# Optimization experiments

Hardware: AMD Instinct MI355X
Metric: run time of the kernel (lower is better)

Reference implementation:

```python
import jax, jax.numpy as jnp
import numpy as np

D_MODEL = 1024
N_HEADS = 16
D_K = D_MODEL // N_HEADS
D_FF = 4096
EPS = 1e-5


def _layernorm(x, g, b):
    mu = jnp.mean(x, axis=-1, keepdims=True)
    var = jnp.var(x, axis=-1, keepdims=True)
    return (x - mu) * jax.lax.rsqrt(var + EPS) * g + b


def setup_inputs() -> dict:
    key = jax.random.key(0)
    ks = jax.random.split(key, 12)
    s = 0.02
    x = jax.random.normal(ks[0], (2, 2048, D_MODEL), dtype=jnp.float32)
    # Linear weights stored [in, out] so y = x @ W + b
    wq = jax.random.normal(ks[1], (D_MODEL, D_MODEL), dtype=jnp.float32) * s
    wk = jax.random.normal(ks[2], (D_MODEL, D_MODEL), dtype=jnp.float32) * s
    wv = jax.random.normal(ks[3], (D_MODEL, D_MODEL), dtype=jnp.float32) * s
    wo = jax.random.normal(ks[4], (D_MODEL, D_MODEL), dtype=jnp.float32) * s
    bq = jnp.zeros((D_MODEL,), jnp.float32)
    bk = jnp.zeros((D_MODEL,), jnp.float32)
    bv = jnp.zeros((D_MODEL,), jnp.float32)
    bo = jnp.zeros((D_MODEL,), jnp.float32)
    ln1_g = jnp.ones((D_MODEL,), jnp.float32)
    ln1_b = jnp.zeros((D_MODEL,), jnp.float32)
    ln2_g = jnp.ones((D_MODEL,), jnp.float32)
    ln2_b = jnp.zeros((D_MODEL,), jnp.float32)
    w1 = jax.random.normal(ks[5], (D_MODEL, D_FF), dtype=jnp.float32) * s
    b1 = jnp.zeros((D_FF,), jnp.float32)
    w2 = jax.random.normal(ks[6], (D_FF, D_MODEL), dtype=jnp.float32) * s
    b2 = jnp.zeros((D_MODEL,), jnp.float32)
    return {"x": x, "wq": wq, "bq": bq, "wk": wk, "bk": bk, "wv": wv, "bv": bv,
            "wo": wo, "bo": bo, "ln1_g": ln1_g, "ln1_b": ln1_b,
            "ln2_g": ln2_g, "ln2_b": ln2_b, "w1": w1, "b1": b1, "w2": w2, "b2": b2}


def reference(x, wq, bq, wk, bk, wv, bv, wo, bo, ln1_g, ln1_b, ln2_g, ln2_b, w1, b1, w2, b2):
    B, S, _ = x.shape
    res = x
    # project and split heads: [B, S, H, Dk]
    q = (x @ wq + bq).reshape(B, S, N_HEADS, D_K)
    k = (x @ wk + bk).reshape(B, S, N_HEADS, D_K)
    v = (x @ wv + bv).reshape(B, S, N_HEADS, D_K)
    # full score matrix [B, H, Sq, Sk] (faithful to unfused original)
    scores = jnp.einsum('bqhd,bkhd->bhqk', q, k) / jnp.sqrt(jnp.float32(D_K))
    weights = jax.nn.softmax(scores, axis=-1)
    attn = jnp.einsum('bhqk,bkhd->bqhd', weights, v).reshape(B, S, D_MODEL)
    x = _layernorm(res + attn @ wo + bo, ln1_g, ln1_b)
    res = x
    h = jax.nn.relu(x @ w1 + b1)
    x = _layernorm(res + h @ w2 + b2, ln2_g, ln2_b)
    return x
```

## Files before the change

kernel.cpp:

```cpp
#include <hip/hip_runtime.h>
#include <hip/hip_bf16.h>
#include <stdint.h>


typedef __hip_bfloat16 bf16;
typedef short bf16x8 __attribute__((ext_vector_type(8)));
typedef float f32x4 __attribute__((ext_vector_type(4)));

#if __has_builtin(__builtin_amdgcn_exp2f)
#define EXP2F(x) __builtin_amdgcn_exp2f(x)
#else
#define EXP2F(x) exp2f(x)
#endif

__device__ __forceinline__ float bf2f_lo(unsigned u) { return __uint_as_float(u << 16); }
__device__ __forceinline__ float bf2f_hi(unsigned u) { return __uint_as_float(u & 0xffff0000u); }
__device__ __forceinline__ ushort f2bf(float f) {
  union { bf16 h; ushort u; } c; c.h = __float2bfloat16(f); return c.u;
}
__device__ __forceinline__ uint pk_bf16(float a, float b) {
  union { __hip_bfloat162 h2; uint u; } c;
  c.h2 = __float22bfloat162_rn(make_float2(a, b));
  return c.u;
}
__device__ __forceinline__ bool is_f32(const uint* probe) { return probe[0] == 0x3F800000u; }
__device__ __forceinline__ float ld_param(const void* p, size_t i, bool f32) {
  return f32 ? ((const float*)p)[i] : __bfloat162float(((const bf16*)p)[i]);
}

template <bool A_EXT, bool RES_EXT>
__device__ __forceinline__ void gemm_body(
    const void* __restrict__ Av, const ushort* __restrict__ BT,
    const void* __restrict__ bias, const void* __restrict__ res,
    void* __restrict__ C, int N_, int K_, int bm, int bn,
    int kb, int ke, int mode, const uint* probe) {
  __shared__ ushort Asm_[128 * 32];
  __shared__ ushort Bsm_[128 * 32];

  const bool F32 = is_f32(probe);
  const bool AF = A_EXT && F32;

  const int tid = threadIdx.x;
  const int wave = tid >> 6;
  const int lane = tid & 63;
  const int wm = wave & 1, wn = wave >> 1;

  const int r0 = tid >> 2;
  const int c0 = (tid & 3) * 8;
  const int dA0 = r0 * 32 + c0;
  const int dA1 = dA0 + 64 * 32;

  const size_t aRow0 = (size_t)(bm * 128 + r0) * K_;
  const size_t aRow1 = aRow0 + (size_t)64 * K_;
  const ushort* pB0 = BT + (size_t)(bn * 128 + r0) * K_ + c0;
  const ushort* pB1 = pB0 + (size_t)64 * K_;

  auto ld4 = [&](int kk, uint4& A0, uint4& A1, uint4& B0, uint4& B1) {
    if (AF) {
      const float* Af = (const float*)Av;
      const float4 f0 = *(const float4*)(Af + aRow0 + kk + c0);
      const float4 f1 = *(const float4*)(Af + aRow0 + kk + c0 + 4);
      const float4 g0 = *(const float4*)(Af + aRow1 + kk + c0);
      const float4 g1 = *(const float4*)(Af + aRow1 + kk + c0 + 4);
      A0.x = pk_bf16(f0.x, f0.y); A0.y = pk_bf16(f0.z, f0.w);
      A0.z = pk_bf16(f1.x, f1.y); A0.w = pk_bf16(f1.z, f1.w);
      A1.x = pk_bf16(g0.x, g0.y); A1.y = pk_bf16(g0.z, g0.w);
      A1.z = pk_bf16(g1.x, g1.y); A1.w = pk_bf16(g1.z, g1.w);
    } else {
      const ushort* Ab = (const ushort*)Av;
      A0 = *(const uint4*)(Ab + aRow0 + kk + c0);
      A1 = *(const uint4*)(Ab + aRow1 + kk + c0);
    }
    B0 = *(const uint4*)(pB0 + kk);
    B1 = *(const uint4*)(pB1 + kk);
  };

  f32x4 zero = {0.f, 0.f, 0.f, 0.f};
  f32x4 acc[4][4];
#pragma unroll
  for (int i = 0; i < 4; ++i)
#pragma unroll
    for (int j = 0; j < 4; ++j) acc[i][j] = zero;

  const int m16 = lane & 15;
  const int quad = lane >> 4;
  const int koff = quad * 8;

  uint4 a0, a1, b0, b1;
  ld4(kb, a0, a1, b0, b1);

  for (int k0 = kb; k0 < ke; k0 += 32) {
    __syncthreads();
    *(uint4*)&Asm_[dA0] = a0;
    *(uint4*)&Asm_[dA1] = a1;
    *(uint4*)&Bsm_[dA0] = b0;
    *(uint4*)&Bsm_[dA1] = b1;
    __syncthreads();

    if (k0 + 32 < ke) ld4(k0 + 32, a0, a1, b0, b1);

    bf16x8 af[4], bfr[4];
#pragma unroll
    for (int i = 0; i < 4; ++i)
      af[i] = *(const bf16x8*)&Asm_[(wm * 64 + i * 16 + m16) * 32 + koff];
#pragma unroll
    for (int j = 0; j < 4; ++j)
      bfr[j] = *(const bf16x8*)&Bsm_[(wn * 64 + j * 16 + m16) * 32 + koff];
#pragma unroll
    for (int i = 0; i < 4; ++i)
#pragma unroll
      for (int j = 0; j < 4; ++j)
        acc[i][j] = __builtin_amdgcn_mfma_f32_16x16x32_bf16(af[i], bfr[j], acc[i][j], 0, 0, 0);
  }

  const int row0 = bm * 128 + wm * 64;
  const int col0 = bn * 128 + wn * 64;
#pragma unroll
  for (int j = 0; j < 4; ++j) {
    const int col = col0 + j * 16 + m16;
    const float bv = (mode == 3) ? 0.f : ld_param(bias, col, F32);
#pragma unroll
    for (int i = 0; i < 4; ++i) {
#pragma unroll
      for (int r = 0; r < 4; ++r) {
        const int row = row0 + i * 16 + quad * 4 + r;
        float v = acc[i][j][r] + bv;
        if (mode == 1) v = fmaxf(v, 0.f);
        if (mode == 2) v += ld_param(res, (size_t)row * N_ + col, RES_EXT && F32);
        if (mode >= 2) ((float*)C)[(size_t)row * N_ + col] = v;
        else ((bf16*)C)[(size_t)row * N_ + col] = __float2bfloat16(v);
      }
    }
  }
}

__global__ __launch_bounds__(256) void gemm_qkv(
    const void* A, const ushort* BT0, const ushort* BT1, const ushort* BT2,
    const void* b0, const void* b1, const void* b2,
    bf16* C0, bf16* C1, bf16* C2, const uint* probe) {
  const int sel = blockIdx.y >> 3, bn = blockIdx.y & 7;
  const ushort* BT = sel == 0 ? BT0 : (sel == 1 ? BT1 : BT2);
  const void* bb = sel == 0 ? b0 : (sel == 1 ? b1 : b2);
  bf16* C = sel == 0 ? C0 : (sel == 1 ? C1 : C2);
  gemm_body<true, false>(A, BT, bb, nullptr, C, 1024, 1024, blockIdx.x, bn,
                         0, 1024, 0, probe);
}
__global__ __launch_bounds__(256) void gemm_wo_sk(
    const ushort* A, const ushort* BT, const void* bias, const void* res,
    float* C0, float* C1, const uint* probe) {
  const int kz = blockIdx.z;
  gemm_body<false, true>(A, BT, bias, res, kz ? C1 : C0, 1024, 1024,
                         blockIdx.x, blockIdx.y, kz * 512, kz * 512 + 512,
                         kz ? 3 : 2, probe);
}
__global__ __launch_bounds__(256) void gemm_ffn1(
    const ushort* A, const ushort* BT, const void* bias, bf16* C, const uint* probe) {
  gemm_body<false, false>(A, BT, bias, nullptr, C, 4096, 1024,
                          blockIdx.x, blockIdx.y, 0, 1024, 1, probe);
}
__global__ __launch_bounds__(256) void gemm_ffn2_sk(
    const ushort* A, const ushort* BT, const void* bias, const ushort* res,
    float* C0, float* C1, const uint* probe) {
  const int kz = blockIdx.z;
  gemm_body<false, false>(A, BT, bias, res, kz ? C1 : C0, 1024, 4096,
                          blockIdx.x, blockIdx.y, kz * 2048, kz * 2048 + 2048,
                          kz ? 3 : 2, probe);
}

__global__ __launch_bounds__(256) void transpose_all(
    const void* W0, const void* W1, const void* W2, const void* W3,
    const void* W4, const void* W5,
    ushort* D0, ushort* D1, ushort* D2, ushort* D3, ushort* D4, ushort* D5,
    const uint* probe) {
  const int z = blockIdx.z;
  if (z < 4 && blockIdx.x >= 32) return;
  int n0, k0, K_, N_;
  const void* W;
  ushort* D;
  if (z < 4) {
    n0 = blockIdx.x * 32; k0 = blockIdx.y * 32; K_ = 1024; N_ = 1024;
    W = z == 0 ? W0 : z == 1 ? W1 : z == 2 ? W2 : W3;
    D = z == 0 ? D0 : z == 1 ? D1 : z == 2 ? D2 : D3;
  } else if (z == 4) {
    n0 = blockIdx.x * 32; k0 = blockIdx.y * 32; K_ = 1024; N_ = 4096; W = W4; D = D4;
  } else {
    n0 = blockIdx.y * 32; k0 = blockIdx.x * 32; K_ = 4096; N_ = 1024; W = W5; D = D5;
  }
  const bool F32 = is_f32(probe);
  __shared__ ushort tile[32][33];
  const int tx = threadIdx.x & 31, ty = threadIdx.x >> 5;
#pragma unroll
  for (int i = 0; i < 32; i += 8) {
    const size_t src = (size_t)(k0 + ty + i) * N_ + n0 + tx;
    tile[ty + i][tx] = F32 ? f2bf(((const float*)W)[src]) : ((const ushort*)W)[src];
  }
  __syncthreads();
#pragma unroll
  for (int i = 0; i < 32; i += 8)
    D[(size_t)(n0 + ty + i) * K_ + k0 + tx] = tile[tx][ty + i];
}

template <bool OUT_EXT>
__global__ __launch_bounds__(256) void ln_kernel(
    const float* __restrict__ X, const float* __restrict__ P,
    const void* __restrict__ g, const void* __restrict__ bta,
    void* __restrict__ out, const uint* probe) {
  const bool F32 = is_f32(probe);
  const int row = blockIdx.x;
  const int tid = threadIdx.x;
  const float4 a = *(const float4*)(X + (size_t)row * 1024 + tid * 4);
  const float4 b = *(const float4*)(P + (size_t)row * 1024 + tid * 4);
  const float xv[4] = {a.x + b.x, a.y + b.y, a.z + b.z, a.w + b.w};
  float s = xv[0] + xv[1] + xv[2] + xv[3];
  float ss = xv[0] * xv[0] + xv[1] * xv[1] + xv[2] * xv[2] + xv[3] * xv[3];
#pragma unroll
  for (int o = 32; o > 0; o >>= 1) { s += __shfl_down(s, o); ss += __shfl_down(ss, o); }
  __shared__ float red[8];
  if ((tid & 63) == 0) { red[tid >> 6] = s; red[4 + (tid >> 6)] = ss; }
  __syncthreads();
  s = red[0] + red[1] + red[2] + red[3];
  ss = red[4] + red[5] + red[6] + red[7];
  const float mu = s * (1.f / 1024.f);
  const float rstd = rsqrtf(ss * (1.f / 1024.f) - mu * mu + 1e-5f);
#pragma unroll
  for (int i = 0; i < 4; ++i) {
    const size_t idx = (size_t)row * 1024 + tid * 4 + i;
    const float y = (xv[i] - mu) * rstd * ld_param(g, tid * 4 + i, F32) +
                    ld_param(bta, tid * 4 + i, F32);
    if (OUT_EXT && F32) ((float*)out)[idx] = y;
    else ((bf16*)out)[idx] = __float2bfloat16(y);
  }
}

__global__ __launch_bounds__(256) void attn_mfma(
    const ushort* __restrict__ Qm, const ushort* __restrict__ Km,
    const ushort* __restrict__ Vm, ushort* __restrict__ Om) {
  __shared__ ushort Ks[64 * 72];
  __shared__ ushort Vt[64 * 72];
  __shared__ ushort Pw[4][32 * 72];

  const int tid = threadIdx.x;
  const int wave = tid >> 6, lane = tid & 63;
  const int m16 = lane & 15, quad = lane >> 4;
  const int bb = blockIdx.z, h = blockIdx.y;
  const size_t hb = ((size_t)bb * 2048) * 1024 + h * 64;
  const int q0 = blockIdx.x * 128 + wave * 32;

  const float QS = 0.125f * 1.44269504f;
  bf16x8 qf[2][2];
#pragma unroll
  for (int i = 0; i < 2; ++i)
#pragma unroll
    for (int c = 0; c < 2; ++c) {
      const uint4 u = *(const uint4*)(Qm + hb + (size_t)(q0 + 16 * i + m16) * 1024 + c * 32 + quad * 8);
      const uint w[4] = {u.x, u.y, u.z, u.w};
      bf16x8 f;
#pragma unroll
      for (int j = 0; j < 4; ++j) {
        const uint p = pk_bf16(bf2f_lo(w[j]) * QS, bf2f_hi(w[j]) * QS);
        f[2 * j]     = (short)(p & 0xffffu);
        f[2 * j + 1] = (short)(p >> 16);
      }
      qf[i][c] = f;
    }

  f32x4 zero = {0.f, 0.f, 0.f, 0.f};
  f32x4 acc[2][4];
#pragma unroll
  for (int i = 0; i < 2; ++i)
#pragma unroll
    for (int j = 0; j < 4; ++j) acc[i][j] = zero;
  float lp[2][4] = {{0.f, 0.f, 0.f, 0.f}, {0.f, 0.f, 0.f, 0.f}};

  const int skey = tid >> 2;
  const int sd = (tid & 3) * 8;
  const int pp = tid & 31;
  const int dc = tid >> 5;
  const int ka_ = 16 * ((2 * pp) & 3) + ((2 * pp) >> 2);
  const int kb_ = 16 * ((2 * pp + 1) & 3) + ((2 * pp + 1) >> 2);
  const ushort* Kg = Km + hb;
  const ushort* Vg = Vm + hb;

  uint4 kr0, kr1, vr0, vr1;
  kr0 = *(const uint4*)(Kg + (size_t)skey * 1024 + sd);
  kr1 = *(const uint4*)(Kg + (size_t)skey * 1024 + sd + 32);
  vr0 = *(const uint4*)(Vg + (size_t)ka_ * 1024 + dc * 8);
  vr1 = *(const uint4*)(Vg + (size_t)kb_ * 1024 + dc * 8);

  for (int kt = 0; kt < 2048; kt += 64) {
    __syncthreads();
    *(uint4*)&Ks[skey * 72 + sd] = kr0;
    *(uint4*)&Ks[skey * 72 + sd + 32] = kr1;
    {
      const uint va[4] = {vr0.x, vr0.y, vr0.z, vr0.w};
      const uint vb[4] = {vr1.x, vr1.y, vr1.z, vr1.w};
#pragma unroll
      for (int j = 0; j < 8; ++j) {
        const uint lo = (j & 1) ? (va[j >> 1] >> 16) : (va[j >> 1] & 0xffffu);
        const uint hi = (j & 1) ? (vb[j >> 1] & 0xffff0000u) : (vb[j >> 1] << 16);
        *(uint*)&Vt[(dc * 8 + j) * 72 + 2 * pp] = lo | hi;
      }
    }
    __syncthreads();

    if (kt + 64 < 2048) {
      kr0 = *(const uint4*)(Kg + (size_t)(kt + 64 + skey) * 1024 + sd);
      kr1 = *(const uint4*)(Kg + (size_t)(kt + 64 + skey) * 1024 + sd + 32);
      vr0 = *(const uint4*)(Vg + (size_t)(kt + 64 + ka_) * 1024 + dc * 8);
      vr1 = *(const uint4*)(Vg + (size_t)(kt + 64 + kb_) * 1024 + dc * 8);
    }

    f32x4 s[2][4];
#pragma unroll
    for (int i = 0; i < 2; ++i)
#pragma unroll
      for (int jn = 0; jn < 4; ++jn) s[i][jn] = zero;
#pragma unroll
    for (int c = 0; c < 2; ++c) {
      bf16x8 kb4[4];
#pragma unroll
      for (int jn = 0; jn < 4; ++jn)
        kb4[jn] = *(const bf16x8*)&Ks[(jn * 16 + m16) * 72 + c * 32 + quad * 8];
#pragma unroll
      for (int i = 0; i < 2; ++i)
#pragma unroll
        for (int jn = 0; jn < 4; ++jn)
          s[i][jn] = __builtin_amdgcn_mfma_f32_16x16x32_bf16(qf[i][c], kb4[jn], s[i][jn], 0, 0, 0);
    }

#pragma unroll
    for (int i = 0; i < 2; ++i)
#pragma unroll
      for (int r = 0; r < 4; ++r) {
        const float p0 = EXP2F(s[i][0][r]);
        const float p1 = EXP2F(s[i][1][r]);
        const float p2 = EXP2F(s[i][2][r]);
        const float p3 = EXP2F(s[i][3][r]);
        lp[i][r] += (p0 + p1) + (p2 + p3);
        uint2 pk;
        pk.x = pk_bf16(p0, p1);
        pk.y = pk_bf16(p2, p3);
        *(uint2*)&Pw[wave][(16 * i + quad * 4 + r) * 72 + m16 * 4] = pk;
      }
    asm volatile("s_waitcnt lgkmcnt(0)" ::: "memory");

#pragma unroll
    for (int c = 0; c < 2; ++c) {
      bf16x8 pa[2], vb4[4];
#pragma unroll
      for (int i = 0; i < 2; ++i)
        pa[i] = *(const bf16x8*)&Pw[wave][(16 * i + m16) * 72 + c * 32 + quad * 8];
#pragma unroll
      for (int jd = 0; jd < 4; ++jd)
        vb4[jd] = *(const bf16x8*)&Vt[(jd * 16 + m16) * 72 + c * 32 + quad * 8];
#pragma unroll
      for (int i = 0; i < 2; ++i)
#pragma unroll
        for (int jd = 0; jd < 4; ++jd)
          acc[i][jd] = __builtin_amdgcn_mfma_f32_16x16x32_bf16(pa[i], vb4[jd], acc[i][jd], 0, 0, 0);
    }
  }

#pragma unroll
  for (int i = 0; i < 2; ++i)
#pragma unroll
    for (int r = 0; r < 4; ++r) {
      float l = lp[i][r];
      l += __shfl_xor(l, 1); l += __shfl_xor(l, 2);
      l += __shfl_xor(l, 4); l += __shfl_xor(l, 8);
      const float inv = 1.f / l;
      const size_t rowoff = hb + (size_t)(q0 + 16 * i + quad * 4 + r) * 1024;
#pragma unroll
      for (int jd = 0; jd < 4; ++jd)
        Om[rowoff + jd * 16 + m16] = f2bf(acc[i][jd][r] * inv);
    }
}

extern "C" void kernel_launch(void* const* d_in, const int* in_sizes, int n_in,
                              void* d_out, int out_size, void* d_ws, size_t ws_size,
                              hipStream_t stream) {
  const void* x   = d_in[0];
  const void* wq  = d_in[1];
  const void* bq  = d_in[2];
  const void* wk  = d_in[3];
  const void* bk  = d_in[4];
  const void* wv  = d_in[5];
  const void* bv  = d_in[6];
  const void* wo  = d_in[7];
  const void* bo  = d_in[8];
  const uint* probe = (const uint*)d_in[9];
  const void* ln1g = d_in[9];
  const void* ln1b = d_in[10];
  const void* ln2g = d_in[11];
  const void* ln2b = d_in[12];
  const void* w1  = d_in[13];
  const void* b1  = d_in[14];
  const void* w2  = d_in[15];
  const void* b2  = d_in[16];

  char* ws = (char*)d_ws;
  const size_t MB = 1ull << 20;
  ushort* wqT = (ushort*)(ws + 0 * MB);
  ushort* wkT = (ushort*)(ws + 2 * MB);
  ushort* wvT = (ushort*)(ws + 4 * MB);
  ushort* woT = (ushort*)(ws + 6 * MB);
  ushort* w1T = (ushort*)(ws + 8 * MB);
  ushort* w2T = (ushort*)(ws + 16 * MB);
  ushort* Qb  = (ushort*)(ws + 24 * MB);
  ushort* Kb  = (ushort*)(ws + 32 * MB);
  ushort* Vb  = (ushort*)(ws + 40 * MB);
  ushort* AO  = (ushort*)(ws + 72 * MB);
  float*  T1  = (float*)(ws + 24 * MB);
  float*  P1w = (float*)(ws + 40 * MB);
  ushort* X1  = (ushort*)(ws + 56 * MB);
  ushort* Hb  = (ushort*)(ws + 24 * MB);
  float*  T1b = (float*)(ws + 0 * MB);
  float*  P1b = (float*)(ws + 64 * MB);

  const dim3 blk(256);
  transpose_all<<<dim3(128, 32, 6), blk, 0, stream>>>(
      wq, wk, wv, wo, w1, w2, wqT, wkT, wvT, woT, w1T, w2T, probe);

  gemm_qkv<<<dim3(32, 24), blk, 0, stream>>>(x, wqT, wkT, wvT, bq, bk, bv,
                                             (bf16*)Qb, (bf16*)Kb, (bf16*)Vb, probe);
  attn_mfma<<<dim3(16, 16, 2), blk, 0, stream>>>(Qb, Kb, Vb, AO);
  gemm_wo_sk<<<dim3(32, 8, 2), blk, 0, stream>>>(AO, woT, bo, x, T1, P1w, probe);
  ln_kernel<false><<<dim3(4096), blk, 0, stream>>>(T1, P1w, ln1g, ln1b, X1, probe);
  gemm_ffn1<<<dim3(32, 32), blk, 0, stream>>>(X1, w1T, b1, (bf16*)Hb, probe);
  gemm_ffn2_sk<<<dim3(32, 8, 2), blk, 0, stream>>>(Hb, w2T, b2, X1, T1b, P1b, probe);
  ln_kernel<true><<<dim3(4096), blk, 0, stream>>>(T1b, P1b, ln2g, ln2b, d_out, probe);
}
```

Measured before the change: 397.9 us.

## Replace 128-tile GEMMs with 256x256 LDS-DMA pipelined GEMM kernel

Adds a 512-thread GEMM that computes a 256x256 output tile per block, stages A/B tiles into double-buffered swizzled LDS via global_load_lds, and interleaves the next-stage loads with MFMA 16x16x32 bursts under raised wave priority. QKV, FFN1 and FFN2 now use it. The QKV input is pre-converted to bf16 by a new convert_x kernel so the GEMM reads only bf16. The larger tiles raise data reuse and the hand pipelining hides load latency. In exchange there are far fewer blocks (e.g. 192 for QKV, 128 for FFN2), which may underfill the CUs, plus one extra launch.

```diff
diff --git a/kernel.cpp b/kernel.cpp
--- a/kernel.cpp
+++ b/kernel.cpp
@@ -26,6 +26,166 @@
 __device__ __forceinline__ bool is_f32(const uint* probe) { return probe[0] == 0x3F800000u; }
 __device__ __forceinline__ float ld_param(const void* p, size_t i, bool f32) {
   return f32 ? ((const float*)p)[i] : __bfloat162float(((const bf16*)p)[i]);
+}
+
+__device__ __forceinline__ void barrier_raw() {
+  asm volatile("" ::: "memory");
+  __builtin_amdgcn_s_barrier();
+  asm volatile("" ::: "memory");
+}
+__device__ __forceinline__ void lgkm0() {
+  asm volatile("s_waitcnt lgkmcnt(0)" ::: "memory");
+}
+__device__ __forceinline__ void glds16(const ushort* g, ushort* l) {
+  __builtin_amdgcn_global_load_lds(
+      (const __attribute__((address_space(1))) void*)g,
+      (__attribute__((address_space(3))) void*)l, 16, 0, 0);
+}
+
+#define MFMA16(MH, NH)                                                        \
+  do {                                                                        \
+    _Pragma("unroll") for (int c_ = 0; c_ < 2; ++c_)                          \
+    _Pragma("unroll") for (int fi_ = 0; fi_ < 4; ++fi_)                       \
+    _Pragma("unroll") for (int gi_ = 0; gi_ < 2; ++gi_)                       \
+      acc[(MH) * 4 + fi_][(NH) * 2 + gi_] =                                   \
+          __builtin_amdgcn_mfma_f32_16x16x32_bf16(                            \
+              areg[fi_][c_], breg[(NH) * 2 + gi_][c_],                        \
+              acc[(MH) * 4 + fi_][(NH) * 2 + gi_], 0, 0, 0);                  \
+  } while (0)
+
+__device__ __forceinline__ void gemm256_body(
+    const ushort* __restrict__ A, const ushort* __restrict__ BT,
+    const void* __restrict__ bias, const void* __restrict__ res,
+    void* __restrict__ C, int N_, int K_, int bm, int bn,
+    int kb, int ke, int mode, const uint* probe) {
+  __shared__ ushort As[2][16384];
+  __shared__ ushort Bs[2][16384];
+
+  const int tid = threadIdx.x;
+  const int wave = tid >> 6;
+  const int lane = tid & 63;
+  const int wm = wave >> 2;
+  const int wn = wave & 3;
+  const int m16 = lane & 15;
+  const int quad = lane >> 4;
+  const int nt = (ke - kb) >> 6;
+
+  const int srow = lane >> 2;
+  const int skc = ((lane & 3) * 8) ^ (((lane >> 5) & 1) << 4);
+  const ushort* pA = A + (size_t)(bm * 256 + wave * 16 + srow) * K_ + kb + skc;
+  const ushort* pB = BT + (size_t)(bn * 256 + wave * 16 + srow) * K_ + kb + skc;
+  const size_t hstep = (size_t)128 * K_;
+  ushort* dA = &As[0][0] + wave * 1024;
+  ushort* dB = &Bs[0][0] + wave * 1024;
+
+  auto stageA = [&](int b, int half, int t) {
+    const ushort* g = pA + (size_t)half * hstep + t * 64;
+    ushort* d = dA + b * 16384 + half * 8192;
+    glds16(g, d);
+    glds16(g + 32, d + 512);
+  };
+  auto stageB = [&](int b, int half, int t) {
+    const ushort* g = pB + (size_t)half * hstep + t * 64;
+    ushort* d = dB + b * 16384 + half * 8192;
+    glds16(g, d);
+    glds16(g + 32, d + 512);
+  };
+
+  const int fr_off = m16 * 32 + ((quad * 8) ^ (((m16 >> 3) & 1) << 4));
+  const ushort* rA = &As[0][0] + fr_off;
+  const ushort* rB = &Bs[0][0] + fr_off;
+  auto ldA = [&](int b, int f, int c) {
+    return *(const bf16x8*)(rA + b * 16384 +
+                            ((f >> 2) * 8 + wm * 4 + (f & 3)) * 1024 + c * 512);
+  };
+  auto ldB = [&](int b, int g, int c) {
+    return *(const bf16x8*)(rB + b * 16384 +
+                            ((g >> 1) * 8 + wn * 2 + (g & 1)) * 1024 + c * 512);
+  };
+
+  f32x4 acc[8][4];
+#pragma unroll
+  for (int f = 0; f < 8; ++f)
+#pragma unroll
+    for (int g = 0; g < 4; ++g) acc[f][g] = (f32x4){0.f, 0.f, 0.f, 0.f};
+  bf16x8 areg[4][2], breg[4][2];
+
+  stageA(0, 0, 0); stageB(0, 0, 0); stageA(0, 1, 0); stageB(0, 1, 0);
+  if (nt > 1) { stageA(1, 0, 1); stageB(1, 0, 1); }
+  asm volatile("s_waitcnt vmcnt(4)" ::: "memory");
+  barrier_raw();
+
+  for (int t = 0; t < nt; ++t) {
+    const int b = t & 1, bo = b ^ 1;
+#pragma unroll
+    for (int fi = 0; fi < 4; ++fi) { areg[fi][0] = ldA(b, fi, 0); areg[fi][1] = ldA(b, fi, 1); }
+#pragma unroll
+    for (int gi = 0; gi < 2; ++gi) { breg[gi][0] = ldB(b, gi, 0); breg[gi][1] = ldB(b, gi, 1); }
+    if (t + 1 < nt) stageA(bo, 1, t + 1);
+    barrier_raw(); lgkm0();
+    __builtin_amdgcn_s_setprio(1); MFMA16(0, 0); __builtin_amdgcn_s_setprio(0);
+    barrier_raw();
+#pragma unroll
+    for (int gi = 2; gi < 4; ++gi) { breg[gi][0] = ldB(b, gi, 0); breg[gi][1] = ldB(b, gi, 1); }
+    if (t + 1 < nt) stageB(bo, 1, t + 1);
+    barrier_raw(); lgkm0();
+    __builtin_amdgcn_s_setprio(1); MFMA16(0, 1); __builtin_amdgcn_s_setprio(0);
+    barrier_raw();
+#pragma unroll
+    for (int fi = 0; fi < 4; ++fi) { areg[fi][0] = ldA(b, fi + 4, 0); areg[fi][1] = ldA(b, fi + 4, 1); }
+    if (t + 2 < nt) stageA(b, 0, t + 2);
+    barrier_raw(); lgkm0();
+    __builtin_amdgcn_s_setprio(1); MFMA16(1, 0); __builtin_amdgcn_s_setprio(0);
+    barrier_raw();
+    if (t + 2 < nt) stageB(b, 0, t + 2);
+    barrier_raw(); lgkm0();
+    __builtin_amdgcn_s_setprio(1); MFMA16(1, 1); __builtin_amdgcn_s_setprio(0);
+    if (t + 2 < nt) asm volatile("s_waitcnt vmcnt(4)" ::: "memory");
+    else            asm volatile("s_waitcnt vmcnt(0)" ::: "memory");
+    barrier_raw();
+  }
+
+  const bool F32 = is_f32(probe);
+#pragma unroll
+  for (int g = 0; g < 4; ++g) {
+    const int col = bn * 256 + (g >> 1) * 128 + wn * 32 + (g & 1) * 16 + m16;
+    const float bv = (mode == 3) ? 0.f : ld_param(bias, col, F32);
+#pragma unroll
+    for (int f = 0; f < 8; ++f) {
+      const int rowb = bm * 256 + (f >> 2) * 128 + wm * 64 + (f & 3) * 16 + quad * 4;
+#pragma unroll
+      for (int r = 0; r < 4; ++r) {
+        const int row = rowb + r;
+        float v = acc[f][g][r] + bv;
+        if (mode == 1) v = fmaxf(v, 0.f);
+        if (mode == 2) v += __bfloat162float(((const bf16*)res)[(size_t)row * N_ + col]);
+        if (mode >= 2) ((float*)C)[(size_t)row * N_ + col] = v;
+        else ((bf16*)C)[(size_t)row * N_ + col] = __float2bfloat16(v);
+      }
+    }
+  }
+}
+
+__global__ __launch_bounds__(512, 2) void gemm256_qkv(
+    const ushort* A, const ushort* BT0, const ushort* BT1, const ushort* BT2,
+    const void* b0, const void* b1, const void* b2,
+    bf16* C0, bf16* C1, bf16* C2, const uint* probe) {
+  const int sel = blockIdx.y >> 2, bn = blockIdx.y & 3;
+  const ushort* BT = sel == 0 ? BT0 : (sel == 1 ? BT1 : BT2);
+  const void* bb = sel == 0 ? b0 : (sel == 1 ? b1 : b2);
+  bf16* C = sel == 0 ? C0 : (sel == 1 ? C1 : C2);
+  gemm256_body(A, BT, bb, nullptr, C, 1024, 1024, blockIdx.x, bn, 0, 1024, 0, probe);
+}
+__global__ __launch_bounds__(512, 2) void gemm256_ffn1(
+    const ushort* A, const ushort* BT, const void* bias, bf16* C, const uint* probe) {
+  gemm256_body(A, BT, bias, nullptr, C, 4096, 1024, blockIdx.x, blockIdx.y, 0, 1024, 1, probe);
+}
+__global__ __launch_bounds__(512, 2) void gemm256_ffn2_sk(
+    const ushort* A, const ushort* BT, const void* bias, const ushort* res,
+    float* C0, float* C1, const uint* probe) {
+  const int kz = blockIdx.z;
+  gemm256_body(A, BT, bias, res, kz ? (void*)C1 : (void*)C0, 1024, 4096,
+               blockIdx.x, blockIdx.y, kz * 2048, kz * 2048 + 2048, kz ? 3 : 2, probe);
 }
 
 template <bool A_EXT, bool RES_EXT>
@@ -134,17 +294,6 @@
   }
 }
 
-__global__ __launch_bounds__(256) void gemm_qkv(
-    const void* A, const ushort* BT0, const ushort* BT1, const ushort* BT2,
-    const void* b0, const void* b1, const void* b2,
-    bf16* C0, bf16* C1, bf16* C2, const uint* probe) {
-  const int sel = blockIdx.y >> 3, bn = blockIdx.y & 7;
-  const ushort* BT = sel == 0 ? BT0 : (sel == 1 ? BT1 : BT2);
-  const void* bb = sel == 0 ? b0 : (sel == 1 ? b1 : b2);
-  bf16* C = sel == 0 ? C0 : (sel == 1 ? C1 : C2);
-  gemm_body<true, false>(A, BT, bb, nullptr, C, 1024, 1024, blockIdx.x, bn,
-                         0, 1024, 0, probe);
-}
 __global__ __launch_bounds__(256) void gemm_wo_sk(
     const ushort* A, const ushort* BT, const void* bias, const void* res,
     float* C0, float* C1, const uint* probe) {
@@ -152,19 +301,6 @@
   gemm_body<false, true>(A, BT, bias, res, kz ? C1 : C0, 1024, 1024,
                          blockIdx.x, blockIdx.y, kz * 512, kz * 512 + 512,
                          kz ? 3 : 2, probe);
-}
-__global__ __launch_bounds__(256) void gemm_ffn1(
-    const ushort* A, const ushort* BT, const void* bias, bf16* C, const uint* probe) {
-  gemm_body<false, false>(A, BT, bias, nullptr, C, 4096, 1024,
-                          blockIdx.x, blockIdx.y, 0, 1024, 1, probe);
-}
-__global__ __launch_bounds__(256) void gemm_ffn2_sk(
-    const ushort* A, const ushort* BT, const void* bias, const ushort* res,
-    float* C0, float* C1, const uint* probe) {
-  const int kz = blockIdx.z;
-  gemm_body<false, false>(A, BT, bias, res, kz ? C1 : C0, 1024, 4096,
-                          blockIdx.x, blockIdx.y, kz * 2048, kz * 2048 + 2048,
-                          kz ? 3 : 2, probe);
 }
 
 __global__ __launch_bounds__(256) void transpose_all(
@@ -198,6 +334,22 @@
 #pragma unroll
   for (int i = 0; i < 32; i += 8)
     D[(size_t)(n0 + ty + i) * K_ + k0 + tx] = tile[tx][ty + i];
+}
+
+__global__ __launch_bounds__(256) void convert_x(
+    const void* __restrict__ X, ushort* __restrict__ out, const uint* probe) {
+  const bool F32 = is_f32(probe);
+  const size_t i = ((size_t)blockIdx.x * 256 + threadIdx.x) * 8;
+  if (F32) {
+    const float4 a = *(const float4*)((const float*)X + i);
+    const float4 b = *(const float4*)((const float*)X + i + 4);
+    uint4 o;
+    o.x = pk_bf16(a.x, a.y); o.y = pk_bf16(a.z, a.w);
+    o.z = pk_bf16(b.x, b.y); o.w = pk_bf16(b.z, b.w);
+    *(uint4*)(out + i) = o;
+  } else {
+    *(uint4*)(out + i) = *(const uint4*)((const ushort*)X + i);
+  }
 }
 
 template <bool OUT_EXT>
@@ -409,6 +561,7 @@
   ushort* Qb  = (ushort*)(ws + 24 * MB);
   ushort* Kb  = (ushort*)(ws + 32 * MB);
   ushort* Vb  = (ushort*)(ws + 40 * MB);
+  ushort* Xb  = (ushort*)(ws + 64 * MB);
   ushort* AO  = (ushort*)(ws + 72 * MB);
   float*  T1  = (float*)(ws + 24 * MB);
   float*  P1w = (float*)(ws + 40 * MB);
@@ -418,15 +571,17 @@
   float*  P1b = (float*)(ws + 64 * MB);
 
   const dim3 blk(256);
+  const dim3 blk512(512);
   transpose_all<<<dim3(128, 32, 6), blk, 0, stream>>>(
       wq, wk, wv, wo, w1, w2, wqT, wkT, wvT, woT, w1T, w2T, probe);
-
-  gemm_qkv<<<dim3(32, 24), blk, 0, stream>>>(x, wqT, wkT, wvT, bq, bk, bv,
-                                             (bf16*)Qb, (bf16*)Kb, (bf16*)Vb, probe);
+  convert_x<<<dim3(2048), blk, 0, stream>>>(x, Xb, probe);
+
+  gemm256_qkv<<<dim3(16, 12), blk512, 0, stream>>>(
+      Xb, wqT, wkT, wvT, bq, bk, bv, (bf16*)Qb, (bf16*)Kb, (bf16*)Vb, probe);
   attn_mfma<<<dim3(16, 16, 2), blk, 0, stream>>>(Qb, Kb, Vb, AO);
   gemm_wo_sk<<<dim3(32, 8, 2), blk, 0, stream>>>(AO, woT, bo, x, T1, P1w, probe);
   ln_kernel<false><<<dim3(4096), blk, 0, stream>>>(T1, P1w, ln1g, ln1b, X1, probe);
-  gemm_ffn1<<<dim3(32, 32), blk, 0, stream>>>(X1, w1T, b1, (bf16*)Hb, probe);
-  gemm_ffn2_sk<<<dim3(32, 8, 2), blk, 0, stream>>>(Hb, w2T, b2, X1, T1b, P1b, probe);
+  gemm256_ffn1<<<dim3(16, 16), blk512, 0, stream>>>(X1, w1T, b1, (bf16*)Hb, probe);
+  gemm256_ffn2_sk<<<dim3(16, 4, 2), blk512, 0, stream>>>(Hb, w2T, b2, X1, T1b, P1b, probe);
   ln_kernel<true><<<dim3(4096), blk, 0, stream>>>(T1b, P1b, ln2g, ln2b, d_out, probe);
 }
```

Result: no change. 399.3 us (+0.4%).
